# Kernel optimization log

Hardware: AMD Instinct MI355X
Metric: run time of the kernel (lower is better)

Reference implementation:

```python
import jax, jax.numpy as jnp
import numpy as np


def setup_inputs() -> dict:
    key = jax.random.key(0)
    ks = jax.random.split(key, 12)
    B, T, D, H = 64, 512, 256, 1024
    s = 0.01
    return {
        "x": jax.random.normal(ks[0], (B, T, D), jnp.float32),
        "Wd": jax.random.normal(ks[1], (D, H), jnp.float32) * s,
        "bd": jax.random.normal(ks[2], (H,), jnp.float32) * s,
        "Wz": jax.random.normal(ks[3], (D, H), jnp.float32) * s,
        "Wr": jax.random.normal(ks[4], (D, H), jnp.float32) * s,
        "Wh": jax.random.normal(ks[5], (D, H), jnp.float32) * s,
        "Uz": jax.random.normal(ks[6], (H, H), jnp.float32) * s,
        "Ur": jax.random.normal(ks[7], (H, H), jnp.float32) * s,
        "Uh": jax.random.normal(ks[8], (H, H), jnp.float32) * s,
        "bz": jax.random.normal(ks[9], (H,), jnp.float32) * s,
        "br": jax.random.normal(ks[10], (H,), jnp.float32) * s,
        "bh": jax.random.normal(ks[11], (H,), jnp.float32) * s,
    }


def reference(x, Wd, bd, Wz, Wr, Wh, Uz, Ur, Uh, bz, br, bh):
    # x: [B, T, D]. GRU-D recurrence with exponential decay of hidden state.
    B, T, D = x.shape
    H = Wd.shape[1]
    # Precompute all input projections in one batched GEMM each: [B, T, H]
    decay_in = jnp.einsum('btd,dh->bth', x, Wd) + bd
    xz = jnp.einsum('btd,dh->bth', x, Wz) + bz
    xr = jnp.einsum('btd,dh->bth', x, Wr) + br
    xh = jnp.einsum('btd,dh->bth', x, Wh) + bh
    gamma = jnp.exp(-jax.nn.relu(decay_in))  # decay factor per step

    def step(h_tm1, inputs):
        g_t, xz_t, xr_t, xh_t = inputs  # each [B, H]
        h_dec = g_t * h_tm1
        z_t = jax.nn.sigmoid(xz_t + h_dec @ Uz)
        r_t = jax.nn.sigmoid(xr_t + h_dec @ Ur)
        h_prop = jnp.tanh(xh_t + (r_t * h_dec) @ Uh)
        h_t = (1.0 - z_t) * h_dec + z_t * h_prop
        return h_t, h_t

    h0 = jnp.zeros((B, H), x.dtype)
    # scan over time: move T to leading axis
    seq = (jnp.swapaxes(gamma, 0, 1), jnp.swapaxes(xz, 0, 1),
           jnp.swapaxes(xr, 0, 1), jnp.swapaxes(xh, 0, 1))
    _, hs = jax.lax.scan(step, h0, seq)  # hs: [T, B, H]
    return jnp.swapaxes(hs, 0, 1)  # [B, T, H]
```

## Files before the change

### kernel.cpp

```cpp
#include <hip/hip_runtime.h>
#include <cstdint>
#include <cstddef>


#define NB 64
#define NT 512
#define ND 256
#define NH 1024

typedef _Float16 h2_t __attribute__((ext_vector_type(2)));
typedef _Float16 half8 __attribute__((ext_vector_type(8)));
typedef float f32x4 __attribute__((ext_vector_type(4)));
typedef uint32_t u32x4 __attribute__((ext_vector_type(4)));

__device__ __forceinline__ uint32_t pack2(float a, float b) {
  h2_t v; v[0] = (_Float16)a; v[1] = (_Float16)b;
  return __builtin_bit_cast(uint32_t, v);
}
__device__ __forceinline__ uint16_t f2h(float x) {
  _Float16 v = (_Float16)x; return __builtin_bit_cast(uint16_t, v);
}
__device__ __forceinline__ float h2f(uint16_t u) {
  return (float)__builtin_bit_cast(_Float16, u);
}
__device__ __forceinline__ float sigm(float x) {
  return 1.f / (1.f + __expf(-x));
}
__device__ __forceinline__ float fast_tanh(float x) {
  float e = __expf(2.f * x);
  return 1.f - 2.f / (e + 1.f);
}
__device__ __forceinline__ float ldnt_h(const uint16_t* p) {
  return h2f(__builtin_nontemporal_load(p));
}
__device__ __forceinline__ void stnt_f(float* p, float v) {
  __builtin_nontemporal_store(v, p);
}

__device__ __forceinline__ u32x4 ld_cg_b128(const uint32_t* p) {
  u32x4 v;
  asm volatile("global_load_dwordx4 %0, %1, off sc0 sc1" : "=v"(v) : "v"(p) : "memory");
  return v;
}
__device__ __forceinline__ void st_cg_b128(uint32_t* p, u32x4 v) {
  asm volatile("global_store_dwordx4 %0, %1, off sc0 sc1" :: "v"(p), "v"(v) : "memory");
}
__device__ __forceinline__ void st_cg_b32(uint32_t* p, unsigned v) {
  asm volatile("global_store_dword %0, %1, off sc0 sc1" :: "v"(p), "v"(v) : "memory");
}
__device__ __forceinline__ unsigned ld_cg_b32w(const uint32_t* p) {
  unsigned v;
  asm volatile("global_load_dword %0, %1, off sc0 sc1\n\ts_waitcnt vmcnt(0)"
               : "=v"(v) : "v"(p) : "memory");
  return v;
}

__global__ __launch_bounds__(256) void transpose_f2h_g(
    const float* __restrict__ src, uint16_t* __restrict__ dst, int R, int C) {
  __shared__ uint16_t lt[64][68];
  int tpc = C >> 6;
  int tr = blockIdx.x / tpc, tc = blockIdx.x % tpc;
  int tid = threadIdx.x;
  int r0 = tid >> 6, cc = tid & 63;
#pragma unroll
  for (int it = 0; it < 16; ++it) {
    int r = it * 4 + r0;
    lt[cc][r] = f2h(src[(size_t)(tr * 64 + r) * C + tc * 64 + cc]);
  }
  __syncthreads();
#pragma unroll
  for (int it = 0; it < 16; ++it) {
    int c = it * 4 + r0;
    dst[(size_t)(tc * 64 + c) * R + tr * 64 + cc] = lt[c][cc];
  }
}

__global__ __launch_bounds__(256) void proj_mfma_k(
    const float* __restrict__ x, const uint16_t* __restrict__ WT,
    const float* __restrict__ bd, const float* __restrict__ bz,
    const float* __restrict__ br, const float* __restrict__ bh,
    uint16_t* __restrict__ g_gamma, uint16_t* __restrict__ g_xz,
    uint16_t* __restrict__ g_xr, uint16_t* __restrict__ g_xh) {
  __shared__ __align__(16) uint16_t As[64][264];
  const int tid = threadIdx.x;
  const int rg = blockIdx.x >> 6;
  const int cg = blockIdx.x & 63;
  const int lane = tid & 63, w = tid >> 6;
  const int r16 = lane & 15, q = lane >> 4;

#pragma unroll
  for (int it = 0; it < 16; ++it) {
    int idx = tid + it * 256;
    int row = idx >> 6, c4 = (idx & 63) << 2;
    float4 v = *(const float4*)(x + (size_t)(rg * 64 + row) * 256 + c4);
    uint32_t* dp = (uint32_t*)&As[row][c4];
    dp[0] = pack2(v.x, v.y);
    dp[1] = pack2(v.z, v.w);
  }
  __syncthreads();

  const int a = cg >> 4;
  const int cbase = (cg & 15) * 64;
  const uint16_t* WTa = WT + (size_t)a * (1024 * 256);
  const float* bias = a == 0 ? bd : a == 1 ? bz : a == 2 ? br : bh;
  uint16_t* dst = a == 0 ? g_gamma : a == 1 ? g_xz : a == 2 ? g_xr : g_xh;
  const bool isg = (a == 0);

  const uint16_t* arow = &As[w * 16 + r16][q * 8];

#pragma unroll
  for (int nt = 0; nt < 4; ++nt) {
    int colg = cbase + nt * 16 + r16;
    const uint16_t* bcol = WTa + (size_t)colg * 256 + q * 8;
    f32x4 acc = {0.f, 0.f, 0.f, 0.f};
#pragma unroll
    for (int kc = 0; kc < 8; ++kc)
      acc = __builtin_amdgcn_mfma_f32_16x16x32_f16(
          *(const half8*)(arow + kc * 32), *(const half8*)(bcol + kc * 32),
          acc, 0, 0, 0);
    float bv = bias[colg];
#pragma unroll
    for (int j = 0; j < 4; ++j) {
      int n = rg * 64 + w * 16 + q * 4 + j;
      int b = n >> 9, t = n & 511;
      float p = acc[j] + bv;
      if (isg) p = __expf(-fmaxf(p, 0.f));
      dst[(((size_t)(t * 64 + b)) << 10) + colg] = f2h(p);
    }
  }
}


__global__ __launch_bounds__(256, 1) void scan_k(
    const uint16_t* __restrict__ UzT, const uint16_t* __restrict__ UrT,
    const uint16_t* __restrict__ UhT,
    const uint16_t* __restrict__ g_gamma, const uint16_t* __restrict__ g_xz,
    const uint16_t* __restrict__ g_xr, const uint16_t* __restrict__ g_xh,
    uint16_t* __restrict__ Hdat, uint16_t* __restrict__ RHdat,
    uint32_t* __restrict__ Htag, uint32_t* __restrict__ RHtag,
    float* __restrict__ out) {
  __shared__ __align__(16) uint16_t Hp[9][1032];
  __shared__ __align__(16) uint16_t RHp[9][1032];
  __shared__ float red[4][4][256];
  __shared__ __align__(16) uint16_t pub16[8][32];

  const int tid = threadIdx.x;
  const int g = blockIdx.x & 7;
  const int slot = blockIdx.x >> 3;
  const int c0 = slot * 32;
  const int lane = tid & 63, w = tid >> 6;
  const int r16 = lane & 15, q = lane >> 4;

  for (int i = tid; i < 1032; i += 256) { Hp[8][i] = 0; RHp[8][i] = 0; }

  half8 Bz[2][8], Br[2][8], Bh[2][8];
#pragma unroll
  for (int ct = 0; ct < 2; ++ct) {
    const size_t colb = (size_t)(c0 + ct * 16 + r16) * 1024 + w * 256 + q * 8;
#pragma unroll
    for (int kc = 0; kc < 8; ++kc) {
      Bz[ct][kc] = *(const half8*)(UzT + colb + kc * 32);
      Br[ct][kc] = *(const half8*)(UrT + colb + kc * 32);
      Bh[ct][kc] = *(const half8*)(UhT + colb + kc * 32);
    }
  }
  __syncthreads();

  const uint16_t* aprow = Hp[r16 < 8 ? r16 : 8];
  const uint16_t* aprow2 = RHp[r16 < 8 ? r16 : 8];
  const int aoff = w * 256 + q * 8;

  const int ect = w & 1;
  const int ecol = c0 + ect * 16 + r16;
  const int erow = q * 4;

  uint32_t* mytagH = Htag + (g * 32 + slot) * 16;
  uint32_t* mytagR = RHtag + (g * 32 + slot) * 16;
  const uint32_t* tagH = Htag + (g * 32 + (tid & 31)) * 16;
  const uint32_t* tagR = RHtag + (g * 32 + (tid & 31)) * 16;

  auto poll_tags = [&](const uint32_t* tp, unsigned exp) {
    for (;;) {
      unsigned v = ld_cg_b32w(tp);
      __builtin_amdgcn_sched_barrier(0);
      if (__all((int)(v == exp))) break;
      __builtin_amdgcn_s_sleep(2);
    }
  };
  auto fill = [&](const uint16_t* dat, uint16_t (&panel)[9][1032]) {
    const uint32_t* src = (const uint32_t*)(dat +
        ((size_t)(g * 8 + (tid >> 5)) << 10) + (size_t)(tid & 31) * 32);
    u32x4 v0 = ld_cg_b128(src);
    u32x4 v1 = ld_cg_b128(src + 4);
    u32x4 v2 = ld_cg_b128(src + 8);
    u32x4 v3 = ld_cg_b128(src + 12);
    asm volatile("s_waitcnt vmcnt(0)" ::: "memory");
    __builtin_amdgcn_sched_barrier(0);
    uint16_t* dst = &panel[tid >> 5][(tid & 31) * 32];
    *(u32x4*)(dst + 0)  = v0;
    *(u32x4*)(dst + 8)  = v1;
    *(u32x4*)(dst + 16) = v2;
    *(u32x4*)(dst + 24) = v3;
  };
  auto publish = [&](uint16_t* dat, uint32_t* tagp, unsigned tagval) {
    if (tid < 32) {
      int r = tid >> 2;
      int cq = (tid & 3) * 8;
      uint32_t* dp = (uint32_t*)(dat + ((size_t)(g * 8 + r) << 10) + c0 + cq);
      st_cg_b128(dp, *(u32x4*)&pub16[r][cq]);
      asm volatile("s_waitcnt vmcnt(0)" ::: "memory");
      if (tid == 0) st_cg_b32(tagp, tagval);
    }
  };

  for (int t = 0; t < NT; ++t) {
    float xzv[4], xrv[4], xhv[4], gmv[4];
    {
      const int tg = (t + 1 < NT) ? t + 1 : t;
#pragma unroll
      for (int j = 0; j < 4; ++j) {
        int rr = erow + j; if (rr > 7) rr = 7;
        size_t base = (((size_t)(t * 64 + g * 8 + rr)) << 10) + ecol;
        if (w < 2) {
          xzv[j] = ldnt_h(&g_xz[base]);
          xhv[j] = ldnt_h(&g_xh[base]);
          gmv[j] = ldnt_h(&g_gamma[(((size_t)(tg * 64 + g * 8 + rr)) << 10) + ecol]);
          xrv[j] = 0.f;
        } else {
          xrv[j] = ldnt_h(&g_xr[base]);
          xzv[j] = xhv[j] = gmv[j] = 0.f;
        }
      }
    }

    poll_tags(tagH, (unsigned)t);
    fill(Hdat, Hp);
    __syncthreads();

    f32x4 az0 = {0.f,0.f,0.f,0.f}, az1 = {0.f,0.f,0.f,0.f};
    f32x4 ar0 = {0.f,0.f,0.f,0.f}, ar1 = {0.f,0.f,0.f,0.f};
#pragma unroll
    for (int kc = 0; kc < 8; ++kc) {
      half8 av = *(const half8*)(aprow + aoff + kc * 32);
      az0 = __builtin_amdgcn_mfma_f32_16x16x32_f16(av, Bz[0][kc], az0, 0, 0, 0);
      az1 = __builtin_amdgcn_mfma_f32_16x16x32_f16(av, Bz[1][kc], az1, 0, 0, 0);
      ar0 = __builtin_amdgcn_mfma_f32_16x16x32_f16(av, Br[0][kc], ar0, 0, 0, 0);
      ar1 = __builtin_amdgcn_mfma_f32_16x16x32_f16(av, Br[1][kc], ar1, 0, 0, 0);
    }
    *(f32x4*)&red[w][0][lane * 4] = az0;
    *(f32x4*)&red[w][1][lane * 4] = az1;
    *(f32x4*)&red[w][2][lane * 4] = ar0;
    *(f32x4*)&red[w][3][lane * 4] = ar1;
    __syncthreads();

    float zk[4] = {0.f,0.f,0.f,0.f}, hdk[4] = {0.f,0.f,0.f,0.f};
    {
      f32x4 s = *(const f32x4*)&red[0][w][lane * 4];
      s += *(const f32x4*)&red[1][w][lane * 4];
      s += *(const f32x4*)&red[2][w][lane * 4];
      s += *(const f32x4*)&red[3][w][lane * 4];
      if (lane < 32) {
        if (w < 2) {
#pragma unroll
          for (int j = 0; j < 4; ++j) {
            zk[j] = sigm(xzv[j] + s[j]);
            hdk[j] = h2f(Hp[erow + j][ecol]);
          }
        } else {
#pragma unroll
          for (int j = 0; j < 4; ++j) {
            float rg = sigm(xrv[j] + s[j]);
            float hd = h2f(Hp[erow + j][ecol]);
            pub16[erow + j][ect * 16 + r16] = f2h(rg * hd);
          }
        }
      }
    }
    __syncthreads();
    publish(RHdat, mytagR, (unsigned)(t + 1));

    poll_tags(tagR, (unsigned)(t + 1));
    fill(RHdat, RHp);
    __syncthreads();

    f32x4 ah0 = {0.f,0.f,0.f,0.f}, ah1 = {0.f,0.f,0.f,0.f};
#pragma unroll
    for (int kc = 0; kc < 8; ++kc) {
      half8 av = *(const half8*)(aprow2 + aoff + kc * 32);
      ah0 = __builtin_amdgcn_mfma_f32_16x16x32_f16(av, Bh[0][kc], ah0, 0, 0, 0);
      ah1 = __builtin_amdgcn_mfma_f32_16x16x32_f16(av, Bh[1][kc], ah1, 0, 0, 0);
    }
    *(f32x4*)&red[w][0][lane * 4] = ah0;
    *(f32x4*)&red[w][1][lane * 4] = ah1;
    __syncthreads();

    if (w < 2) {
      f32x4 s = *(const f32x4*)&red[0][w][lane * 4];
      s += *(const f32x4*)&red[1][w][lane * 4];
      s += *(const f32x4*)&red[2][w][lane * 4];
      s += *(const f32x4*)&red[3][w][lane * 4];
      if (lane < 32) {
#pragma unroll
        for (int j = 0; j < 4; ++j) {
          float hp = fast_tanh(xhv[j] + s[j]);
          float h = (1.f - zk[j]) * hdk[j] + zk[j] * hp;
          int b = g * 8 + erow + j;
          stnt_f(&out[((size_t)b * NT + t) * NH + ecol], h);
          pub16[erow + j][ect * 16 + r16] = f2h(gmv[j] * h);
        }
      }
    }
    __syncthreads();
    if (t + 1 < NT) publish(Hdat, mytagH, (unsigned)(t + 1));
  }
}


extern "C" void kernel_launch(void* const* d_in, const int* in_sizes, int n_in,
                              void* d_out, int out_size, void* d_ws, size_t ws_size,
                              hipStream_t stream) {
  const float* x  = (const float*)d_in[0];
  const float* Wd = (const float*)d_in[1];
  const float* bd = (const float*)d_in[2];
  const float* Wz = (const float*)d_in[3];
  const float* Wr = (const float*)d_in[4];
  const float* Wh = (const float*)d_in[5];
  const float* Uz = (const float*)d_in[6];
  const float* Ur = (const float*)d_in[7];
  const float* Uh = (const float*)d_in[8];
  const float* bz = (const float*)d_in[9];
  const float* br = (const float*)d_in[10];
  const float* bh = (const float*)d_in[11];
  float* out = (float*)d_out;

  char* ws = (char*)d_ws;
  size_t off = 0;
  auto take = [&](size_t bytes) -> char* {
    char* p = ws + off;
    off = (off + bytes + 255) & ~(size_t)255;
    return p;
  };
  uint16_t* WT  = (uint16_t*)take((size_t)4 * 1024 * 256 * 2);
  uint16_t* UzT = (uint16_t*)take((size_t)1024 * 1024 * 2);
  uint16_t* UrT = (uint16_t*)take((size_t)1024 * 1024 * 2);
  uint16_t* UhT = (uint16_t*)take((size_t)1024 * 1024 * 2);
  uint16_t* g_gamma = (uint16_t*)take((size_t)NT * NB * NH * 2);
  uint16_t* g_xz   = (uint16_t*)take((size_t)NT * NB * NH * 2);
  uint16_t* g_xr   = (uint16_t*)take((size_t)NT * NB * NH * 2);
  uint16_t* g_xh   = (uint16_t*)take((size_t)NT * NB * NH * 2);
  uint16_t* Hdat   = (uint16_t*)take((size_t)NB * NH * 2);
  uint16_t* RHdat  = (uint16_t*)take((size_t)NB * NH * 2);
  uint32_t* Htag   = (uint32_t*)take((size_t)8 * 32 * 16 * 4);
  uint32_t* RHtag  = (uint32_t*)take((size_t)8 * 32 * 16 * 4);
  (void)ws_size; (void)in_sizes; (void)n_in; (void)out_size;

  (void)hipMemsetAsync(Hdat, 0, (size_t)NB * NH * 2, stream);
  (void)hipMemsetAsync(Htag, 0, (size_t)8 * 32 * 16 * 4, stream);
  (void)hipMemsetAsync(RHtag, 0, (size_t)8 * 32 * 16 * 4, stream);

  transpose_f2h_g<<<64, 256, 0, stream>>>(Wd, WT + 0 * (1024 * 256), 256, 1024);
  transpose_f2h_g<<<64, 256, 0, stream>>>(Wz, WT + 1 * (1024 * 256), 256, 1024);
  transpose_f2h_g<<<64, 256, 0, stream>>>(Wr, WT + 2 * (1024 * 256), 256, 1024);
  transpose_f2h_g<<<64, 256, 0, stream>>>(Wh, WT + 3 * (1024 * 256), 256, 1024);
  transpose_f2h_g<<<256, 256, 0, stream>>>(Uz, UzT, 1024, 1024);
  transpose_f2h_g<<<256, 256, 0, stream>>>(Ur, UrT, 1024, 1024);
  transpose_f2h_g<<<256, 256, 0, stream>>>(Uh, UhT, 1024, 1024);

  proj_mfma_k<<<512 * 64, 256, 0, stream>>>(x, WT, bd, bz, br, bh,
                                            g_gamma, g_xz, g_xr, g_xh);

  scan_k<<<256, 256, 0, stream>>>(UzT, UrT, UhT, g_gamma, g_xz, g_xr, g_xh,
                                  Hdat, RHdat, Htag, RHtag, out);
}
```

Baseline: 3.721 ms.

## Restructure LDS layouts for conflict-free reduction, coalesced fill, and deferred output stores

The cross-wave reduction buffer changes from vector-per-lane storage to a component-major layout, so each scalar store and load is lane-contiguous and avoids LDS bank conflicts. The panel fill now has consecutive threads load consecutive 16-byte chunks, which coalesces the global reads and the LDS writes. Output values are staged in shared memory, and the idle waves write them to global memory after the hidden-state publish, taking the output stores off the recurrence's critical path. The cost is more LDS space and more scalar LDS instructions per step.

```diff
diff --git a/kernel.cpp b/kernel.cpp
--- a/kernel.cpp
+++ b/kernel.cpp
@@ -141,8 +141,9 @@
     float* __restrict__ out) {
   __shared__ __align__(16) uint16_t Hp[9][1032];
   __shared__ __align__(16) uint16_t RHp[9][1032];
-  __shared__ float red[4][4][256];
+  __shared__ float red[4][4][4][256];
   __shared__ __align__(16) uint16_t pub16[8][32];
+  __shared__ float outs[8][32];
 
   const int tid = threadIdx.x;
   const int g = blockIdx.x & 7;
@@ -188,19 +189,21 @@
     }
   };
   auto fill = [&](const uint16_t* dat, uint16_t (&panel)[9][1032]) {
-    const uint32_t* src = (const uint32_t*)(dat +
-        ((size_t)(g * 8 + (tid >> 5)) << 10) + (size_t)(tid & 31) * 32);
-    u32x4 v0 = ld_cg_b128(src);
-    u32x4 v1 = ld_cg_b128(src + 4);
-    u32x4 v2 = ld_cg_b128(src + 8);
-    u32x4 v3 = ld_cg_b128(src + 12);
+    u32x4 v[4];
+#pragma unroll
+    for (int it = 0; it < 4; ++it) {
+      int c = it * 256 + tid;
+      const uint32_t* src = (const uint32_t*)(dat +
+          ((size_t)(g * 8 + (c >> 7)) << 10) + (size_t)(c & 127) * 8);
+      v[it] = ld_cg_b128(src);
+    }
     asm volatile("s_waitcnt vmcnt(0)" ::: "memory");
     __builtin_amdgcn_sched_barrier(0);
-    uint16_t* dst = &panel[tid >> 5][(tid & 31) * 32];
-    *(u32x4*)(dst + 0)  = v0;
-    *(u32x4*)(dst + 8)  = v1;
-    *(u32x4*)(dst + 16) = v2;
-    *(u32x4*)(dst + 24) = v3;
+#pragma unroll
+    for (int it = 0; it < 4; ++it) {
+      int c = it * 256 + tid;
+      *(u32x4*)&panel[c >> 7][(c & 127) * 8] = v[it];
+    }
   };
   auto publish = [&](uint16_t* dat, uint32_t* tagp, unsigned tagval) {
     if (tid < 32) {
@@ -247,18 +250,22 @@
       ar0 = __builtin_amdgcn_mfma_f32_16x16x32_f16(av, Br[0][kc], ar0, 0, 0, 0);
       ar1 = __builtin_amdgcn_mfma_f32_16x16x32_f16(av, Br[1][kc], ar1, 0, 0, 0);
     }
-    *(f32x4*)&red[w][0][lane * 4] = az0;
-    *(f32x4*)&red[w][1][lane * 4] = az1;
-    *(f32x4*)&red[w][2][lane * 4] = ar0;
-    *(f32x4*)&red[w][3][lane * 4] = ar1;
+#pragma unroll
+    for (int k = 0; k < 4; ++k) {
+      red[w][0][k][lane] = az0[k];
+      red[w][1][k][lane] = az1[k];
+      red[w][2][k][lane] = ar0[k];
+      red[w][3][k][lane] = ar1[k];
+    }
     __syncthreads();
 
     float zk[4] = {0.f,0.f,0.f,0.f}, hdk[4] = {0.f,0.f,0.f,0.f};
     {
-      f32x4 s = *(const f32x4*)&red[0][w][lane * 4];
-      s += *(const f32x4*)&red[1][w][lane * 4];
-      s += *(const f32x4*)&red[2][w][lane * 4];
-      s += *(const f32x4*)&red[3][w][lane * 4];
+      f32x4 s;
+#pragma unroll
+      for (int k = 0; k < 4; ++k)
+        s[k] = red[0][w][k][lane] + red[1][w][k][lane] +
+               red[2][w][k][lane] + red[3][w][k][lane];
       if (lane < 32) {
         if (w < 2) {
 #pragma unroll
@@ -290,28 +297,40 @@
       ah0 = __builtin_amdgcn_mfma_f32_16x16x32_f16(av, Bh[0][kc], ah0, 0, 0, 0);
       ah1 = __builtin_amdgcn_mfma_f32_16x16x32_f16(av, Bh[1][kc], ah1, 0, 0, 0);
     }
-    *(f32x4*)&red[w][0][lane * 4] = ah0;
-    *(f32x4*)&red[w][1][lane * 4] = ah1;
+#pragma unroll
+    for (int k = 0; k < 4; ++k) {
+      red[w][0][k][lane] = ah0[k];
+      red[w][1][k][lane] = ah1[k];
+    }
     __syncthreads();
 
     if (w < 2) {
-      f32x4 s = *(const f32x4*)&red[0][w][lane * 4];
-      s += *(const f32x4*)&red[1][w][lane * 4];
-      s += *(const f32x4*)&red[2][w][lane * 4];
-      s += *(const f32x4*)&red[3][w][lane * 4];
+      f32x4 s;
+#pragma unroll
+      for (int k = 0; k < 4; ++k)
+        s[k] = red[0][w][k][lane] + red[1][w][k][lane] +
+               red[2][w][k][lane] + red[3][w][k][lane];
       if (lane < 32) {
 #pragma unroll
         for (int j = 0; j < 4; ++j) {
           float hp = fast_tanh(xhv[j] + s[j]);
           float h = (1.f - zk[j]) * hdk[j] + zk[j] * hp;
-          int b = g * 8 + erow + j;
-          stnt_f(&out[((size_t)b * NT + t) * NH + ecol], h);
+          outs[erow + j][ect * 16 + r16] = h;
           pub16[erow + j][ect * 16 + r16] = f2h(gmv[j] * h);
         }
       }
     }
     __syncthreads();
     if (t + 1 < NT) publish(Hdat, mytagH, (unsigned)(t + 1));
+    if (w >= 2) {
+      int idx = tid - 128;
+#pragma unroll
+      for (int k = 0; k < 2; ++k) {
+        int ii = idx * 2 + k;
+        int r = ii >> 5, cc = ii & 31;
+        stnt_f(&out[((size_t)(g * 8 + r) * NT + t) * NH + c0 + cc], outs[r][cc]);
+      }
+    }
   }
 }
 
```

After: 3.463 ms. 1.07x faster.
